# Kernel optimization log

Hardware: AMD Instinct MI355X
Metric: run time of the kernel (lower is better)

Reference implementation:

```python
import jax, jax.numpy as jnp
import numpy as np

N_NODES = 100000
N_EDGES = 1600000
IN_CH = 64
OUT_CH = 64
N_CLASSES = 10


def setup_inputs() -> dict:
    key = jax.random.key(0)
    k1, k2, k3, k4 = jax.random.split(key, 4)
    x = jax.random.normal(k1, (N_NODES, IN_CH), dtype=jnp.float32)
    edge_index = jax.random.randint(k2, (2, N_EDGES), 0, N_NODES, dtype=jnp.int64)
    # Glorot-scaled weights like PyG GCNConv init
    W1 = jax.random.normal(k3, (IN_CH, OUT_CH), dtype=jnp.float32) * (1.0 / np.sqrt(IN_CH))
    b1 = jnp.zeros((OUT_CH,), dtype=jnp.float32)
    W2 = jax.random.normal(k4, (OUT_CH, N_CLASSES), dtype=jnp.float32) * (1.0 / np.sqrt(OUT_CH))
    b2 = jnp.zeros((N_CLASSES,), dtype=jnp.float32)
    return {"x": x, "W1": W1, "b1": b1, "W2": W2, "b2": b2, "edge_index": edge_index}


def _gcn_conv(x, W, b, src, dst, num_nodes):
    """PyG GCNConv: out = D^{-1/2} (A + I) D^{-1/2} (x W) + b."""
    h = x @ W  # [N, F_out] -- project first (PyG order)
    loops = jnp.arange(num_nodes, dtype=src.dtype)
    s = jnp.concatenate([src, loops])  # message sources j
    d = jnp.concatenate([dst, loops])  # message targets i
    deg = jax.ops.segment_sum(jnp.ones(s.shape, h.dtype), d, num_segments=num_nodes)
    deg_inv_sqrt = jnp.where(deg > 0, jax.lax.rsqrt(jnp.maximum(deg, 1.0)), 0.0)
    norm = deg_inv_sqrt[s] * deg_inv_sqrt[d]  # [E+N]
    msg = h[s] * norm[:, None]  # gather + normalize
    out = jax.ops.segment_sum(msg, d, num_segments=num_nodes)  # scatter-add
    return out + b


def reference(x, W1, b1, W2, b2, edge_index):
    src, dst = edge_index[0], edge_index[1]
    n = x.shape[0]
    h = _gcn_conv(x, W1, b1, src, dst, n)
    out = _gcn_conv(h, W2, b2, src, dst, n)
    return out
```

## Files before the change

kernel.cpp:

```cpp
#include <hip/hip_runtime.h>
#include <hip/hip_fp16.h>


#define NN 100000
#define NE 1600000
#define NPB 256
#define NB 391
#define CHUNK 4096
#define NCB 391
#define MAXB 5120

__global__ __launch_bounds__(256) void k_part(const int* __restrict__ src,
                                              const int* __restrict__ dst,
                                              const float* __restrict__ W1,
                                              const float* __restrict__ W2,
                                              const float* __restrict__ b1,
                                              int* __restrict__ packed,
                                              int* __restrict__ scanT,
                                              float* __restrict__ W12,
                                              float* __restrict__ c1) {
    __shared__ int hist[NB];
    __shared__ int sc[256];
    __shared__ int cur[NB];
    __shared__ int buf[CHUNK];
    int c = blockIdx.x, t = threadIdx.x;
    if (c == NCB) {
        for (int o = t; o < 640; o += 256) {
            int k = o / 10, ch = o - k * 10;
            float acc = 0.f;
            #pragma unroll
            for (int m = 0; m < 64; ++m) acc = fmaf(W1[k * 64 + m], W2[m * 10 + ch], acc);
            W12[o] = acc;
        }
        if (t < 10) {
            float acc = 0.f;
            #pragma unroll
            for (int m = 0; m < 64; ++m) acc = fmaf(b1[m], W2[m * 10 + t], acc);
            c1[t] = acc;
        }
        return;
    }
    int e0 = c * CHUNK, e1 = min(e0 + CHUNK, NE);
    int n = e1 - e0;
    for (int i = t; i < NB; i += 256) hist[i] = 0;
    __syncthreads();
    int pk[16], bk[16];
    #pragma unroll
    for (int k = 0; k < 16; ++k) {
        int e = e0 + t + k * 256;
        if (e < e1) {
            int s = src[e], d = dst[e];
            pk[k] = (s << 8) | (d & 255);
            bk[k] = d >> 8;
            atomicAdd(&hist[bk[k]], 1);
        } else bk[k] = -1;
    }
    __syncthreads();
    int i0 = 2 * t, i1 = 2 * t + 1;
    int h0 = (i0 < NB) ? hist[i0] : 0;
    int h1 = (i1 < NB) ? hist[i1] : 0;
    int ps = h0 + h1;
    sc[t] = ps; __syncthreads();
    for (int off = 1; off < 256; off <<= 1) {
        int a = (t >= off) ? sc[t - off] : 0;
        __syncthreads(); sc[t] += a; __syncthreads();
    }
    int exc = sc[t] - ps;
    if (i0 < NB) cur[i0] = exc;
    if (i1 < NB) cur[i1] = exc + h0;
    __syncthreads();
    for (int b = t; b < NB; b += 256) scanT[c * (NB + 1) + b] = e0 + cur[b];
    if (t == 0) scanT[c * (NB + 1) + NB] = e0 + n;
    __syncthreads();
    #pragma unroll
    for (int k = 0; k < 16; ++k) {
        if (bk[k] >= 0) {
            int pos = atomicAdd(&cur[bk[k]], 1);
            buf[pos] = pk[k];
        }
    }
    __syncthreads();
    for (int i = t; i < n; i += 256) packed[e0 + i] = buf[i];
}

__global__ __launch_bounds__(512) void k_sortproj(const int* __restrict__ packed,
                                                  const int* __restrict__ scanT,
                                                  const float* __restrict__ x,
                                                  const float* __restrict__ W12g,
                                                  int* __restrict__ ssrc,
                                                  int2* __restrict__ rowbe,
                                                  float* __restrict__ dis,
                                                  uint2* __restrict__ ydu) {
    __shared__ int stage[MAXB];
    __shared__ int cnt[NPB];
    __shared__ int sc[NPB];
    __shared__ int cur[NPB];
    __shared__ float disl[NPB];
    __shared__ float Wl[640];
    __shared__ int stot;
    int b = blockIdx.x, t = threadIdx.x;

    if (t < NPB) cnt[t] = 0;
    if (t == 0) stot = 0;
    __syncthreads();
    for (int c = t; c < NCB; c += 512) {
        int s0 = scanT[c * (NB + 1) + b];
        int s1 = scanT[c * (NB + 1) + b + 1];
        int m = s1 - s0;
        if (m > 0) {
            int o = atomicAdd(&stot, m);
            int j = s0;
            while ((j & 3) && j < s1) {
                int p = packed[j++];
                if (o < MAXB) stage[o] = p;
                ++o;
                atomicAdd(&cnt[p & 255], 1);
            }
            for (; j + 3 < s1; j += 4) {
                int4 v = *(const int4*)&packed[j];
                if (o + 3 < MAXB) {
                    stage[o + 0] = v.x; stage[o + 1] = v.y;
                    stage[o + 2] = v.z; stage[o + 3] = v.w;
                }
                o += 4;
                atomicAdd(&cnt[v.x & 255], 1);
                atomicAdd(&cnt[v.y & 255], 1);
                atomicAdd(&cnt[v.z & 255], 1);
                atomicAdd(&cnt[v.w & 255], 1);
            }
            for (; j < s1; ++j) {
                int p = packed[j];
                if (o < MAXB) stage[o] = p;
                ++o;
                atomicAdd(&cnt[p & 255], 1);
            }
        }
    }
    __syncthreads();
    int T = min(stot, MAXB);
    if (t < NPB) sc[t] = cnt[t];
    __syncthreads();
    for (int off = 1; off < NPB; off <<= 1) {
        int a = 0;
        if (t < NPB && t >= off) a = sc[t - off];
        __syncthreads();
        if (t < NPB) sc[t] += a;
        __syncthreads();
    }
    if (t < NPB) {
        int h = cnt[t];
        int exc = sc[t] - h;
        int wbase = b * MAXB;
        int nidx = b * NPB + t;
        float dh = rsqrtf((float)h + 1.0f);
        disl[t] = dh;
        if (nidx < NN) {
            rowbe[nidx] = make_int2(wbase + min(exc, MAXB), wbase + min(exc + h, MAXB));
            dis[nidx] = dh;
        }
        cur[t] = wbase + exc;
    }
    for (int i = t; i < 640; i += 512) Wl[i] = W12g[i];
    __syncthreads();
    {
        int wlim = b * MAXB + MAXB;
        for (int i = t; i < T; i += 512) {
            int p = stage[i];
            int pos = atomicAdd(&cur[p & 255], 1);
            if (pos < wlim) ssrc[pos] = p >> 8;
        }
    }
    __syncthreads();

    int r = t >> 1, h = t & 1;
    int n = b * NPB + r;
    if (n < NN) {
        const float* xr = &x[n * 64 + h * 32];
        float4 xa[8];
        #pragma unroll
        for (int i = 0; i < 8; ++i) xa[i] = *(const float4*)&xr[i * 4];
        float acc[10];
        #pragma unroll
        for (int ch = 0; ch < 10; ++ch) acc[ch] = 0.f;
        #pragma unroll
        for (int i = 0; i < 8; ++i) {
            int k0 = h * 32 + i * 4;
            #pragma unroll
            for (int ch = 0; ch < 10; ++ch) {
                acc[ch] = fmaf(xa[i].x, Wl[(k0 + 0) * 10 + ch], acc[ch]);
                acc[ch] = fmaf(xa[i].y, Wl[(k0 + 1) * 10 + ch], acc[ch]);
                acc[ch] = fmaf(xa[i].z, Wl[(k0 + 2) * 10 + ch], acc[ch]);
                acc[ch] = fmaf(xa[i].w, Wl[(k0 + 3) * 10 + ch], acc[ch]);
            }
        }
        #pragma unroll
        for (int ch = 0; ch < 10; ++ch) acc[ch] += __shfl_xor(acc[ch], 1);
        float dh = disl[r];
        if (h == 0) {
            __half2 p0 = __floats2half2_rn(dh * acc[0], dh * acc[1]);
            __half2 p1 = __floats2half2_rn(dh * acc[2], dh * acc[3]);
            uint2 w; w.x = *(unsigned*)&p0; w.y = *(unsigned*)&p1;
            ydu[n * 4 + 0] = w;
        } else {
            __half2 p0 = __floats2half2_rn(dh * acc[4], dh * acc[5]);
            __half2 p1 = __floats2half2_rn(dh * acc[6], dh * acc[7]);
            uint2 w; w.x = *(unsigned*)&p0; w.y = *(unsigned*)&p1;
            ydu[n * 4 + 1] = w;
            __half2 p2 = __floats2half2_rn(dh * acc[8], dh * acc[9]);
            __half2 p3 = __floats2half2_rn(dh, 0.f);
            uint2 w2; w2.x = *(unsigned*)&p2; w2.y = *(unsigned*)&p3;
            ydu[n * 4 + 2] = w2;
        }
    }
}

__device__ __forceinline__ float4 cvt4(uint2 v) {
    __half2 h0 = *(__half2*)&v.x, h1 = *(__half2*)&v.y;
    float2 f0 = __half22float2(h0), f1 = __half22float2(h1);
    return make_float4(f0.x, f0.y, f1.x, f1.y);
}

__global__ __launch_bounds__(256) void k_aggA(const uint2* __restrict__ ydu,
                                              const float* __restrict__ dis,
                                              const int2* __restrict__ rowbe,
                                              const int* __restrict__ ssrc,
                                              uint2* __restrict__ zdu) {
    int t = blockIdx.x * blockDim.x + threadIdx.x;
    int n = t >> 2, q = t & 3;
    if (n >= NN) return;
    int2 be = rowbe[n];
    const bool act = (q < 3);
    float4 a0 = make_float4(0.f, 0.f, 0.f, 0.f), a1 = a0, a2 = a0, a3 = a0;
    if (act) a0 = cvt4(ydu[n * 4 + q]);
    int j = be.x;
    for (; j + 3 < be.y; j += 4) {
        int s0 = ssrc[j], s1 = ssrc[j + 1], s2 = ssrc[j + 2], s3 = ssrc[j + 3];
        if (act) {
            float4 v0 = cvt4(ydu[s0 * 4 + q]);
            float4 v1 = cvt4(ydu[s1 * 4 + q]);
            float4 v2 = cvt4(ydu[s2 * 4 + q]);
            float4 v3 = cvt4(ydu[s3 * 4 + q]);
            a0.x += v0.x; a0.y += v0.y; a0.z += v0.z; a0.w += v0.w;
            a1.x += v1.x; a1.y += v1.y; a1.z += v1.z; a1.w += v1.w;
            a2.x += v2.x; a2.y += v2.y; a2.z += v2.z; a2.w += v2.w;
            a3.x += v3.x; a3.y += v3.y; a3.z += v3.z; a3.w += v3.w;
        }
    }
    for (; j < be.y; ++j) {
        int s = ssrc[j];
        if (act) {
            float4 v = cvt4(ydu[s * 4 + q]);
            a0.x += v.x; a0.y += v.y; a0.z += v.z; a0.w += v.w;
        }
    }
    if (act) {
        float4 s;
        s.x = (a0.x + a1.x) + (a2.x + a3.x);
        s.y = (a0.y + a1.y) + (a2.y + a3.y);
        s.z = (a0.z + a1.z) + (a2.z + a3.z);
        s.w = (a0.w + a1.w) + (a2.w + a3.w);
        float d = dis[n], d2 = d * d;
        __half2 lo, hi;
        if (q < 2) {
            lo = __floats2half2_rn(d2 * s.x, d2 * s.y);
            hi = __floats2half2_rn(d2 * s.z, d2 * s.w);
        } else {
            lo = __floats2half2_rn(d2 * s.x, d2 * s.y);
            hi = __floats2half2_rn(d * s.z, 0.f);
        }
        uint2 w; w.x = *(unsigned*)&lo; w.y = *(unsigned*)&hi;
        zdu[n * 4 + q] = w;
    }
}

__global__ __launch_bounds__(256) void k_aggB(const uint2* __restrict__ zdu,
                                              const float* __restrict__ dis,
                                              const int2* __restrict__ rowbe,
                                              const int* __restrict__ ssrc,
                                              const float* __restrict__ c1,
                                              const float* __restrict__ b2,
                                              float* __restrict__ out) {
    int t = blockIdx.x * blockDim.x + threadIdx.x;
    int n = t >> 2, q = t & 3;
    if (n >= NN) return;
    int2 be = rowbe[n];
    const bool act = (q < 3);
    float4 self = make_float4(0.f, 0.f, 0.f, 0.f);
    if (act) self = cvt4(zdu[n * 4 + q]);
    float4 a0 = self, a1 = make_float4(0.f, 0.f, 0.f, 0.f), a2 = a1, a3 = a1;
    int j = be.x;
    for (; j + 3 < be.y; j += 4) {
        int s0 = ssrc[j], s1 = ssrc[j + 1], s2 = ssrc[j + 2], s3 = ssrc[j + 3];
        if (act) {
            float4 v0 = cvt4(zdu[s0 * 4 + q]);
            float4 v1 = cvt4(zdu[s1 * 4 + q]);
            float4 v2 = cvt4(zdu[s2 * 4 + q]);
            float4 v3 = cvt4(zdu[s3 * 4 + q]);
            a0.x += v0.x; a0.y += v0.y; a0.z += v0.z; a0.w += v0.w;
            a1.x += v1.x; a1.y += v1.y; a1.z += v1.z; a1.w += v1.w;
            a2.x += v2.x; a2.y += v2.y; a2.z += v2.z; a2.w += v2.w;
            a3.x += v3.x; a3.y += v3.y; a3.z += v3.z; a3.w += v3.w;
        }
    }
    for (; j < be.y; ++j) {
        int s = ssrc[j];
        if (act) {
            float4 v = cvt4(zdu[s * 4 + q]);
            a0.x += v.x; a0.y += v.y; a0.z += v.z; a0.w += v.w;
        }
    }
    float4 s;
    s.x = (a0.x + a1.x) + (a2.x + a3.x);
    s.y = (a0.y + a1.y) + (a2.y + a3.y);
    s.z = (a0.z + a1.z) + (a2.z + a3.z);
    s.w = (a0.w + a1.w) + (a2.w + a3.w);
    float n1 = __shfl(self.z, 2, 4);
    float d = dis[n];
    if (q == 0) {
        out[n * 10 + 0] = fmaf(d, s.x, fmaf(n1, c1[0], b2[0]));
        out[n * 10 + 1] = fmaf(d, s.y, fmaf(n1, c1[1], b2[1]));
        out[n * 10 + 2] = fmaf(d, s.z, fmaf(n1, c1[2], b2[2]));
        out[n * 10 + 3] = fmaf(d, s.w, fmaf(n1, c1[3], b2[3]));
    } else if (q == 1) {
        out[n * 10 + 4] = fmaf(d, s.x, fmaf(n1, c1[4], b2[4]));
        out[n * 10 + 5] = fmaf(d, s.y, fmaf(n1, c1[5], b2[5]));
        out[n * 10 + 6] = fmaf(d, s.z, fmaf(n1, c1[6], b2[6]));
        out[n * 10 + 7] = fmaf(d, s.w, fmaf(n1, c1[7], b2[7]));
    } else if (q == 2) {
        out[n * 10 + 8] = fmaf(d, s.x, fmaf(n1, c1[8], b2[8]));
        out[n * 10 + 9] = fmaf(d, s.y, fmaf(n1, c1[9], b2[9]));
    }
}

extern "C" void kernel_launch(void* const* d_in, const int* in_sizes, int n_in,
                              void* d_out, int out_size, void* d_ws, size_t ws_size,
                              hipStream_t stream) {
    const float* x  = (const float*)d_in[0];
    const float* W1 = (const float*)d_in[1];
    const float* b1 = (const float*)d_in[2];
    const float* W2 = (const float*)d_in[3];
    const float* b2 = (const float*)d_in[4];
    const int* edge = (const int*)d_in[5];
    const int* src = edge;
    const int* dst = edge + NE;
    float* out = (float*)d_out;

    char* W = (char*)d_ws;
    uint2* ydu    = (uint2*)(W);
    uint2* zdu    = (uint2*)(W + 3200000);
    float* dis    = (float*)(W + 6400000);
    int*   packed = (int*)  (W + 6800000);
    int*   scanT  = (int*)  (W + 13200000);
    int*   ssrc   = (int*)  (W + 13813120);
    int2*  rowbe  = (int2*) (W + 21820800);
    float* W12    = (float*)(W + 22620800);
    float* c1     = (float*)(W + 22623360);

    k_part    <<<NCB + 1, 256, 0, stream>>>(src, dst, W1, W2, b1, packed, scanT, W12, c1);
    k_sortproj<<<NB, 512, 0, stream>>>(packed, scanT, x, W12, ssrc, rowbe, dis, ydu);
    k_aggA    <<<(NN * 4 + 255) / 256, 256, 0, stream>>>(ydu, dis, rowbe, ssrc, zdu);
    k_aggB    <<<(NN * 4 + 255) / 256, 256, 0, stream>>>(zdu, dis, rowbe, ssrc, c1, b2, out);
}
```

Measured before the change: 74.33 us.

## Load bucket segments via scanned offsets and stage sorted output in shared memory

Replaces the per-thread segment walk (each of 391 threads reading one variable-length chunk segment) with a block-wide prefix scan of segment lengths and a binary search per element. All 512 threads then read packed elements with coalesced, balanced work. The counting-sort scatter now writes into a shared-memory buffer, and the result is written to global ssrc in one coalesced sequential pass. This costs extra shared memory (about 20KB more), a 9-step scan, and a binary search per element, which may reduce occupancy.

```diff
diff --git a/kernel.cpp b/kernel.cpp
--- a/kernel.cpp
+++ b/kernel.cpp
@@ -92,52 +92,49 @@
                                                   float* __restrict__ dis,
                                                   uint2* __restrict__ ydu) {
     __shared__ int stage[MAXB];
+    __shared__ int sorted[MAXB];
+    __shared__ int sstart[NCB];
+    __shared__ int segoff[NCB + 1];
+    __shared__ int sc512[512];
     __shared__ int cnt[NPB];
     __shared__ int sc[NPB];
     __shared__ int cur[NPB];
     __shared__ float disl[NPB];
     __shared__ float Wl[640];
-    __shared__ int stot;
     int b = blockIdx.x, t = threadIdx.x;
+    int wbase = b * MAXB;
 
     if (t < NPB) cnt[t] = 0;
-    if (t == 0) stot = 0;
-    __syncthreads();
-    for (int c = t; c < NCB; c += 512) {
-        int s0 = scanT[c * (NB + 1) + b];
-        int s1 = scanT[c * (NB + 1) + b + 1];
-        int m = s1 - s0;
-        if (m > 0) {
-            int o = atomicAdd(&stot, m);
-            int j = s0;
-            while ((j & 3) && j < s1) {
-                int p = packed[j++];
-                if (o < MAXB) stage[o] = p;
-                ++o;
-                atomicAdd(&cnt[p & 255], 1);
-            }
-            for (; j + 3 < s1; j += 4) {
-                int4 v = *(const int4*)&packed[j];
-                if (o + 3 < MAXB) {
-                    stage[o + 0] = v.x; stage[o + 1] = v.y;
-                    stage[o + 2] = v.z; stage[o + 3] = v.w;
-                }
-                o += 4;
-                atomicAdd(&cnt[v.x & 255], 1);
-                atomicAdd(&cnt[v.y & 255], 1);
-                atomicAdd(&cnt[v.z & 255], 1);
-                atomicAdd(&cnt[v.w & 255], 1);
-            }
-            for (; j < s1; ++j) {
-                int p = packed[j];
-                if (o < MAXB) stage[o] = p;
-                ++o;
-                atomicAdd(&cnt[p & 255], 1);
-            }
-        }
-    }
-    __syncthreads();
-    int T = min(stot, MAXB);
+    int myl = 0;
+    if (t < NCB) {
+        int s0 = scanT[t * (NB + 1) + b];
+        int s1 = scanT[t * (NB + 1) + b + 1];
+        sstart[t] = s0;
+        myl = s1 - s0;
+    }
+    sc512[t] = myl;
+    __syncthreads();
+    for (int off = 1; off < 512; off <<= 1) {
+        int a = (t >= off) ? sc512[t - off] : 0;
+        __syncthreads(); sc512[t] += a; __syncthreads();
+    }
+    if (t < NCB) segoff[t] = sc512[t] - myl;
+    if (t == 0) segoff[NCB] = sc512[511];
+    __syncthreads();
+    int Tfull = sc512[511];
+    int T = min(Tfull, MAXB);
+
+    for (int i = t; i < Tfull; i += 512) {
+        int lo = 0, hi = NCB;
+        while (hi - lo > 1) {
+            int mid = (lo + hi) >> 1;
+            if (segoff[mid] <= i) lo = mid; else hi = mid;
+        }
+        int p = packed[sstart[lo] + (i - segoff[lo])];
+        if (i < MAXB) stage[i] = p;
+        atomicAdd(&cnt[p & 255], 1);
+    }
+    __syncthreads();
     if (t < NPB) sc[t] = cnt[t];
     __syncthreads();
     for (int off = 1; off < NPB; off <<= 1) {
@@ -150,7 +147,6 @@
     if (t < NPB) {
         int h = cnt[t];
         int exc = sc[t] - h;
-        int wbase = b * MAXB;
         int nidx = b * NPB + t;
         float dh = rsqrtf((float)h + 1.0f);
         disl[t] = dh;
@@ -158,18 +154,17 @@
             rowbe[nidx] = make_int2(wbase + min(exc, MAXB), wbase + min(exc + h, MAXB));
             dis[nidx] = dh;
         }
-        cur[t] = wbase + exc;
+        cur[t] = exc;
     }
     for (int i = t; i < 640; i += 512) Wl[i] = W12g[i];
     __syncthreads();
-    {
-        int wlim = b * MAXB + MAXB;
-        for (int i = t; i < T; i += 512) {
-            int p = stage[i];
-            int pos = atomicAdd(&cur[p & 255], 1);
-            if (pos < wlim) ssrc[pos] = p >> 8;
-        }
-    }
+    for (int i = t; i < T; i += 512) {
+        int p = stage[i];
+        int pos = atomicAdd(&cur[p & 255], 1);
+        if (pos < MAXB) sorted[pos] = p;
+    }
+    __syncthreads();
+    for (int i = t; i < T; i += 512) ssrc[wbase + i] = sorted[i] >> 8;
     __syncthreads();
 
     int r = t >> 1, h = t & 1;
```

New measurement: 72.50 us. -2.5%, faster.
